# Kernel tuning notes

Hardware: AMD Instinct MI355X
Metric: run time of the kernel (lower is better)

Reference implementation:

```python
import jax, jax.numpy as jnp
import numpy as np

N_NODES = 50000
N_EDGES = 800000
D = 128
L = 4
N_GRAPHS = 512
N_CLASSES = 10
BN_EPS = 1e-5


def setup_inputs() -> dict:
    key = jax.random.key(0)
    ks = jax.random.split(key, 8)
    x = jax.random.normal(ks[0], (N_NODES, D), dtype=jnp.float32)
    W = jax.random.normal(ks[1], (L, D, D), dtype=jnp.float32) * (1.0 / np.sqrt(D))
    b = jnp.zeros((L, D), dtype=jnp.float32)
    gamma = jnp.ones((L, D), dtype=jnp.float32)
    beta = jnp.zeros((L, D), dtype=jnp.float32)
    Wc = jax.random.normal(ks[2], (D, N_CLASSES), dtype=jnp.float32) * (1.0 / np.sqrt(D))
    bc = jnp.zeros((N_CLASSES,), dtype=jnp.float32)
    edge_index = jax.random.randint(ks[3], (2, N_EDGES), 0, N_NODES, dtype=jnp.int64)
    batch = jnp.sort(jax.random.randint(ks[4], (N_NODES,), 0, N_GRAPHS, dtype=jnp.int64))
    return {"x": x, "W": W, "b": b, "gamma": gamma, "beta": beta,
            "Wc": Wc, "bc": bc, "edge_index": edge_index, "batch": batch}


def _gcn_conv(x, W_l, b_l, src, dst, deg_inv, norm):
    # h = x @ W, then symmetric-normalized aggregation with self-loops (PyG GCNConv)
    h = x @ W_l                                            # [N, D]
    msg = h[src] * norm[:, None]                           # [E, D] gather + scale
    agg = jax.ops.segment_sum(msg, dst, num_segments=N_NODES)  # scatter-add
    agg = agg + h * (deg_inv * deg_inv)[:, None]           # self-loop term: deg^-1 * h_i
    return agg + b_l


def reference(x, W, b, gamma, beta, Wc, bc, edge_index, batch):
    src, dst = edge_index[0], edge_index[1]
    # degree with self-loops (edge_weight = 1), computed at target nodes
    deg = jax.ops.segment_sum(jnp.ones((N_EDGES,), x.dtype), dst, num_segments=N_NODES) + 1.0
    deg_inv = deg ** -0.5                                  # [N]
    norm = deg_inv[src] * deg_inv[dst]                     # [E]
    for l in range(L):
        x = _gcn_conv(x, W[l], b[l], src, dst, deg_inv, norm)
        # BatchNorm1d (training-mode statistics, biased variance) + ReLU
        mu = jnp.mean(x, axis=0)
        var = jnp.mean((x - mu) ** 2, axis=0)
        x = (x - mu) * jax.lax.rsqrt(var + BN_EPS) * gamma[l] + beta[l]
        x = jax.nn.relu(x)
        # dropout omitted (eval-mode / deterministic reference)
    # global mean pool over graphs, then classifier
    sums = jax.ops.segment_sum(x, batch, num_segments=N_GRAPHS)          # [G, D]
    counts = jax.ops.segment_sum(jnp.ones((N_NODES,), x.dtype), batch, num_segments=N_GRAPHS)
    pooled = sums / jnp.maximum(counts, 1.0)[:, None]
    return pooled @ Wc + bc                                # [G, num_classes]
```

## Files before the change

kernel.cpp:

```cpp
#include <hip/hip_runtime.h>
#include <hip/hip_bf16.h>

#define N_NODES 50000
#define N_EDGES 800000
#define D 128
#define NLAYERS 4
#define N_GRAPHS 512
#define N_CLASSES 10
#define BN_EPS 1e-5f
#define SCAN_BLOCKS ((N_NODES + 1023) / 1024)
#define NPART 64

__global__ void k_hist(const int* __restrict__ ei, int* __restrict__ counts) {
    int e = blockIdx.x * blockDim.x + threadIdx.x;
    if (e < N_EDGES) atomicAdd(&counts[ei[N_EDGES + e]], 1);
}

__global__ __launch_bounds__(1024) void k_scan1(const int* __restrict__ counts,
                                                int* __restrict__ offsets,
                                                float* __restrict__ deg_inv,
                                                int* __restrict__ bsum) {
    __shared__ int wsum[16];
    int tid = threadIdx.x, lane = tid & 63, wid = tid >> 6;
    int i = blockIdx.x * 1024 + tid;
    int v = (i < N_NODES) ? counts[i] : 0;
    if (i < N_NODES) deg_inv[i] = rsqrtf((float)v + 1.0f);
    int x = v;
    #pragma unroll
    for (int off = 1; off < 64; off <<= 1) {
        int y = __shfl_up(x, off, 64);
        if (lane >= off) x += y;
    }
    if (lane == 63) wsum[wid] = x;
    __syncthreads();
    if (wid == 0 && lane < 16) {
        int w = wsum[lane];
        #pragma unroll
        for (int off = 1; off < 16; off <<= 1) {
            int y = __shfl_up(w, off, 16);
            if (lane >= off) w += y;
        }
        wsum[lane] = w;
    }
    __syncthreads();
    int wbase = (wid > 0) ? wsum[wid - 1] : 0;
    int incl = x + wbase;
    if (i < N_NODES) offsets[i + 1] = incl;
    if (tid == 1023) bsum[blockIdx.x] = incl;
}

__global__ __launch_bounds__(1024) void k_scan2(int* __restrict__ offsets,
                                                const int* __restrict__ bsum) {
    __shared__ int s_pre;
    int b = blockIdx.x, tid = threadIdx.x;
    if (tid == 0) {
        int p = 0;
        for (int j = 0; j < b; j++) p += bsum[j];
        s_pre = p;
        if (b == 0) offsets[0] = 0;
    }
    __syncthreads();
    int i = b * 1024 + tid;
    if (i < N_NODES) offsets[i + 1] += s_pre;
}

__global__ void k_scatter(const int* __restrict__ ei, const int* __restrict__ offsets,
                          int* __restrict__ cursor, const float* __restrict__ deg_inv,
                          int2* __restrict__ csr) {
    int e = blockIdx.x * blockDim.x + threadIdx.x;
    if (e >= N_EDGES) return;
    int s = ei[e];
    int d = ei[N_EDGES + e];
    int pos = offsets[d] + atomicAdd(&cursor[d], 1);
    csr[pos] = make_int2(s, __float_as_int(deg_inv[s] * deg_inv[d]));
}

#define GEMM_BM 64
__global__ __launch_bounds__(256) void k_gemm(const float* __restrict__ X,
                                              const float* __restrict__ Wl,
                                              float* __restrict__ H,
                                              const float* __restrict__ gstats,
                                              const float* __restrict__ gamma,
                                              const float* __restrict__ beta,
                                              int do_bn_relu) {
    __shared__ float xs[GEMM_BM][D];
    __shared__ float s_sc[D], s_sh[D];
    int tid = threadIdx.x;
    if (tid < D) {
        if (do_bn_relu) {
            float s = 0.f, q = 0.f;
            #pragma unroll 8
            for (int p = 0; p < NPART; p++) {
                s += gstats[p * 2 * D + tid];
                q += gstats[p * 2 * D + D + tid];
            }
            const float invN = 1.0f / (float)N_NODES;
            float mu = s * invN;
            float var = q * invN - mu * mu;
            float sc = gamma[tid] * rsqrtf(var + BN_EPS);
            s_sc[tid] = sc;
            s_sh[tid] = beta[tid] - mu * sc;
        } else {
            s_sc[tid] = 1.0f;
            s_sh[tid] = 0.0f;
        }
    }
    __syncthreads();
    int row0 = blockIdx.x * GEMM_BM;
    #pragma unroll
    for (int j = 0; j < 8; j++) {
        int idx = tid + j * 256;
        int r = idx >> 5;
        int c4 = (idx & 31) * 4;
        float4 v;
        int gr = row0 + r;
        if (gr < N_NODES) v = *(const float4*)&X[(long)gr * D + c4];
        else v = make_float4(0.f, 0.f, 0.f, 0.f);
        if (do_bn_relu) {
            v.x = fmaxf(v.x * s_sc[c4 + 0] + s_sh[c4 + 0], 0.f);
            v.y = fmaxf(v.y * s_sc[c4 + 1] + s_sh[c4 + 1], 0.f);
            v.z = fmaxf(v.z * s_sc[c4 + 2] + s_sh[c4 + 2], 0.f);
            v.w = fmaxf(v.w * s_sc[c4 + 3] + s_sh[c4 + 3], 0.f);
        }
        *(float4*)&xs[r][c4] = v;
    }
    __syncthreads();
    int tc = tid & 31, tr = tid >> 5;
    int r0 = tr * 8, c0 = tc * 4;
    float acc[8][4] = {};
    #pragma unroll 4
    for (int k = 0; k < D; k++) {
        float4 w = *(const float4*)&Wl[k * D + c0];
        #pragma unroll
        for (int i = 0; i < 8; i++) {
            float xv = xs[r0 + i][k];
            acc[i][0] += xv * w.x;
            acc[i][1] += xv * w.y;
            acc[i][2] += xv * w.z;
            acc[i][3] += xv * w.w;
        }
    }
    #pragma unroll
    for (int i = 0; i < 8; i++) {
        int gr = row0 + r0 + i;
        if (gr < N_NODES) {
            float4 o = make_float4(acc[i][0], acc[i][1], acc[i][2], acc[i][3]);
            *(float4*)&H[(long)gr * D + c0] = o;
        }
    }
}

#define AGG_NPW 2
#define AGG_WAVES 4
#define AGG_NPB (AGG_NPW * AGG_WAVES)
__global__ __launch_bounds__(256) void k_agg(const float* __restrict__ H,
                                             const float* __restrict__ deg_inv,
                                             const int* __restrict__ offsets,
                                             const int2* __restrict__ csr,
                                             const float* __restrict__ bias,
                                             float* __restrict__ Xout,
                                             float* __restrict__ gstats) {
    __shared__ float s_sum[D], s_sq[D];
    int tid = threadIdx.x, lane = tid & 63, wid = tid >> 6;
    if (tid < D) { s_sum[tid] = 0.f; s_sq[tid] = 0.f; }
    __syncthreads();
    int c = lane * 2;
    float b0 = bias[c], b1 = bias[c + 1];
    float ps0 = 0.f, ps1 = 0.f, pq0 = 0.f, pq1 = 0.f;
    int nodeBase = blockIdx.x * AGG_NPB + wid * AGG_NPW;
    for (int t = 0; t < AGG_NPW; t++) {
        int n = nodeBase + t;
        if (n >= N_NODES) break;
        float di = deg_inv[n];
        float2 hv = *(const float2*)&H[(long)n * D + c];
        float self = di * di;
        float a0 = hv.x * self + b0;
        float a1 = hv.y * self + b1;
        int e = offsets[n], e1 = offsets[n + 1];
        for (; e + 4 <= e1; e += 4) {
            int2 p0 = csr[e + 0];
            int2 p1 = csr[e + 1];
            int2 p2 = csr[e + 2];
            int2 p3 = csr[e + 3];
            float2 h0 = *(const float2*)&H[(long)p0.x * D + c];
            float2 h1 = *(const float2*)&H[(long)p1.x * D + c];
            float2 h2 = *(const float2*)&H[(long)p2.x * D + c];
            float2 h3 = *(const float2*)&H[(long)p3.x * D + c];
            float w0 = __int_as_float(p0.y), w1 = __int_as_float(p1.y);
            float w2 = __int_as_float(p2.y), w3 = __int_as_float(p3.y);
            a0 += h0.x * w0; a1 += h0.y * w0;
            a0 += h1.x * w1; a1 += h1.y * w1;
            a0 += h2.x * w2; a1 += h2.y * w2;
            a0 += h3.x * w3; a1 += h3.y * w3;
        }
        for (; e < e1; e++) {
            int2 p = csr[e];
            float w = __int_as_float(p.y);
            float2 hs = *(const float2*)&H[(long)p.x * D + c];
            a0 += hs.x * w;
            a1 += hs.y * w;
        }
        *(float2*)&Xout[(long)n * D + c] = make_float2(a0, a1);
        ps0 += a0; ps1 += a1;
        pq0 += a0 * a0; pq1 += a1 * a1;
    }
    atomicAdd(&s_sum[c], ps0);
    atomicAdd(&s_sum[c + 1], ps1);
    atomicAdd(&s_sq[c], pq0);
    atomicAdd(&s_sq[c + 1], pq1);
    __syncthreads();
    if (tid < D) {
        int part = blockIdx.x & (NPART - 1);
        float* gp = gstats + (size_t)part * 2 * D;
        atomicAdd(&gp[tid], s_sum[tid]);
        atomicAdd(&gp[D + tid], s_sq[tid]);
    }
}

__global__ __launch_bounds__(256) void k_poolcls(const float* __restrict__ X,
                                                 const int* __restrict__ batch,
                                                 const float* __restrict__ gstats,
                                                 const float* __restrict__ gamma,
                                                 const float* __restrict__ beta,
                                                 const float* __restrict__ Wc,
                                                 const float* __restrict__ bc,
                                                 float* __restrict__ out) {
    __shared__ float s_pool[D];
    __shared__ float s_sc[D], s_sh[D];
    __shared__ int s_lo, s_hi;
    int g = blockIdx.x, tid = threadIdx.x;
    if (tid == 0) {
        int lo = 0, hi = N_NODES;
        while (lo < hi) { int m = (lo + hi) >> 1; if (batch[m] < g) lo = m + 1; else hi = m; }
        s_lo = lo;
        hi = N_NODES;
        while (lo < hi) { int m = (lo + hi) >> 1; if (batch[m] < g + 1) lo = m + 1; else hi = m; }
        s_hi = lo;
    }
    if (tid < D) {
        float s = 0.f, q = 0.f;
        #pragma unroll 8
        for (int p = 0; p < NPART; p++) {
            s += gstats[p * 2 * D + tid];
            q += gstats[p * 2 * D + D + tid];
        }
        const float invN = 1.0f / (float)N_NODES;
        float mu = s * invN;
        float var = q * invN - mu * mu;
        float sc = gamma[tid] * rsqrtf(var + BN_EPS);
        s_sc[tid] = sc;
        s_sh[tid] = beta[tid] - mu * sc;
        s_pool[tid] = 0.f;
    }
    __syncthreads();
    int lo = s_lo, hi = s_hi;
    int c4 = (tid & 31) * 4, q = tid >> 5;
    float sc[4], sh[4];
    #pragma unroll
    for (int j = 0; j < 4; j++) { sc[j] = s_sc[c4 + j]; sh[j] = s_sh[c4 + j]; }
    float acc[4] = {0.f, 0.f, 0.f, 0.f};
    for (int n = lo + q; n < hi; n += 8) {
        float4 v = *(const float4*)&X[(long)n * D + c4];
        acc[0] += fmaxf(v.x * sc[0] + sh[0], 0.f);
        acc[1] += fmaxf(v.y * sc[1] + sh[1], 0.f);
        acc[2] += fmaxf(v.z * sc[2] + sh[2], 0.f);
        acc[3] += fmaxf(v.w * sc[3] + sh[3], 0.f);
    }
    #pragma unroll
    for (int j = 0; j < 4; j++) atomicAdd(&s_pool[c4 + j], acc[j]);
    __syncthreads();
    if (tid < N_CLASSES) {
        float cnt = fmaxf((float)(hi - lo), 1.0f);
        float r = 0.f;
        #pragma unroll 16
        for (int k = 0; k < D; k++) r += s_pool[k] * Wc[k * N_CLASSES + tid];
        out[(long)g * N_CLASSES + tid] = r / cnt + bc[tid];
    }
}

extern "C" void kernel_launch(void* const* d_in, const int* in_sizes, int n_in,
                              void* d_out, int out_size, void* d_ws, size_t ws_size,
                              hipStream_t stream) {
    const float* x     = (const float*)d_in[0];
    const float* W     = (const float*)d_in[1];
    const float* b     = (const float*)d_in[2];
    const float* gamma = (const float*)d_in[3];
    const float* beta  = (const float*)d_in[4];
    const float* Wc    = (const float*)d_in[5];
    const float* bc    = (const float*)d_in[6];
    const int*   ei    = (const int*)d_in[7];
    const int*   batch = (const int*)d_in[8];
    float* out = (float*)d_out;

    char* ws = (char*)d_ws;
    size_t off = 0;
    auto alloc = [&](size_t bytes) {
        void* p = ws + off;
        off += (bytes + 255) & ~(size_t)255;
        return p;
    };
    float* cur_x    = (float*)alloc((size_t)N_NODES * D * 4);
    float* h        = (float*)alloc((size_t)N_NODES * D * 4);
    float* deg_inv  = (float*)alloc(N_NODES * 4);
    int*   offsets  = (int*)alloc((N_NODES + 1) * 4);
    int2*  csr      = (int2*)alloc((size_t)N_EDGES * 8);
    int*   bsum     = (int*)alloc(SCAN_BLOCKS * 4);
    size_t zero_begin = off;
    int*   counts   = (int*)alloc(N_NODES * 4);
    int*   cursor   = (int*)alloc(N_NODES * 4);
    float* gstats   = (float*)alloc((size_t)NLAYERS * NPART * 2 * D * 4);
    size_t zero_end = off;

    hipMemsetAsync(ws + zero_begin, 0, zero_end - zero_begin, stream);

    k_hist<<<(N_EDGES + 255) / 256, 256, 0, stream>>>(ei, counts);
    k_scan1<<<SCAN_BLOCKS, 1024, 0, stream>>>(counts, offsets, deg_inv, bsum);
    k_scan2<<<SCAN_BLOCKS, 1024, 0, stream>>>(offsets, bsum);
    k_scatter<<<(N_EDGES + 255) / 256, 256, 0, stream>>>(ei, offsets, cursor, deg_inv, csr);

    const int gemm_grid = (N_NODES + GEMM_BM - 1) / GEMM_BM;
    const int agg_grid = (N_NODES + AGG_NPB - 1) / AGG_NPB;
    const size_t lstat = (size_t)NPART * 2 * D;
    for (int l = 0; l < NLAYERS; l++) {
        const float* Xin = (l == 0) ? x : cur_x;
        const float* st  = (l == 0) ? nullptr : gstats + (size_t)(l - 1) * lstat;
        const float* gm  = gamma + (size_t)((l == 0) ? 0 : l - 1) * D;
        const float* bt  = beta + (size_t)((l == 0) ? 0 : l - 1) * D;
        k_gemm<<<gemm_grid, 256, 0, stream>>>(Xin, W + (size_t)l * D * D, h,
                                              st, gm, bt, (l == 0) ? 0 : 1);
        k_agg<<<agg_grid, 256, 0, stream>>>(h, deg_inv, offsets, csr,
                                            b + (size_t)l * D, cur_x,
                                            gstats + (size_t)l * lstat);
    }

    k_poolcls<<<N_GRAPHS, 256, 0, stream>>>(cur_x, batch,
                                            gstats + (size_t)(NLAYERS - 1) * lstat,
                                            gamma + (size_t)(NLAYERS - 1) * D,
                                            beta + (size_t)(NLAYERS - 1) * D,
                                            Wc, bc, out);
}
```

Measured before the change: 633.9 us.

## Store H in column-chunked layout and aggregate per feature chunk

The GEMM now writes H as 8 column chunks of 16 features, each stored contiguously per node. Aggregation blocks handle one chunk, with a wave splitting edges across 4 slots and combining them by shuffle reduction, so each chunk (3.2 MB) is more likely to stay cache-resident during the random gathers. The cost is that each CSR row is re-read once per chunk, and each gather only fetches 64 bytes per edge. The grid assumes N_NODES is divisible by 16, and the node bounds check has been removed.

```diff
diff --git a/kernel.cpp b/kernel.cpp
--- a/kernel.cpp
+++ b/kernel.cpp
@@ -10,6 +10,8 @@
 #define BN_EPS 1e-5f
 #define SCAN_BLOCKS ((N_NODES + 1023) / 1024)
 #define NPART 64
+#define NCHUNK 8
+#define CHUNKW 16
 
 __global__ void k_hist(const int* __restrict__ ei, int* __restrict__ counts) {
     int e = blockIdx.x * blockDim.x + threadIdx.x;
@@ -78,7 +80,7 @@
 #define GEMM_BM 64
 __global__ __launch_bounds__(256) void k_gemm(const float* __restrict__ X,
                                               const float* __restrict__ Wl,
-                                              float* __restrict__ H,
+                                              float* __restrict__ Hc,
                                               const float* __restrict__ gstats,
                                               const float* __restrict__ gamma,
                                               const float* __restrict__ beta,
@@ -140,80 +142,82 @@
             acc[i][3] += xv * w.w;
         }
     }
+    int chunk = c0 >> 4;
+    int within = c0 & 15;
     #pragma unroll
     for (int i = 0; i < 8; i++) {
         int gr = row0 + r0 + i;
         if (gr < N_NODES) {
             float4 o = make_float4(acc[i][0], acc[i][1], acc[i][2], acc[i][3]);
-            *(float4*)&H[(long)gr * D + c0] = o;
-        }
-    }
-}
-
-#define AGG_NPW 2
-#define AGG_WAVES 4
-#define AGG_NPB (AGG_NPW * AGG_WAVES)
-__global__ __launch_bounds__(256) void k_agg(const float* __restrict__ H,
+            *(float4*)&Hc[(size_t)chunk * N_NODES * CHUNKW + (size_t)gr * CHUNKW + within] = o;
+        }
+    }
+}
+
+#define AGGC_NPW 4
+#define AGGC_WAVES 4
+#define AGGC_NPB (AGGC_NPW * AGGC_WAVES)
+__global__ __launch_bounds__(256) void k_agg(const float* __restrict__ Hc,
                                              const float* __restrict__ deg_inv,
                                              const int* __restrict__ offsets,
                                              const int2* __restrict__ csr,
                                              const float* __restrict__ bias,
                                              float* __restrict__ Xout,
                                              float* __restrict__ gstats) {
-    __shared__ float s_sum[D], s_sq[D];
+    __shared__ float s_sum[CHUNKW], s_sq[CHUNKW];
     int tid = threadIdx.x, lane = tid & 63, wid = tid >> 6;
-    if (tid < D) { s_sum[tid] = 0.f; s_sq[tid] = 0.f; }
-    __syncthreads();
-    int c = lane * 2;
-    float b0 = bias[c], b1 = bias[c + 1];
-    float ps0 = 0.f, ps1 = 0.f, pq0 = 0.f, pq1 = 0.f;
-    int nodeBase = blockIdx.x * AGG_NPB + wid * AGG_NPW;
-    for (int t = 0; t < AGG_NPW; t++) {
-        int n = nodeBase + t;
-        if (n >= N_NODES) break;
-        float di = deg_inv[n];
-        float2 hv = *(const float2*)&H[(long)n * D + c];
-        float self = di * di;
-        float a0 = hv.x * self + b0;
-        float a1 = hv.y * self + b1;
+    int bid = blockIdx.x;
+    int chunk = bid & (NCHUNK - 1);
+    int grp = bid >> 3;
+    if (tid < CHUNKW) { s_sum[tid] = 0.f; s_sq[tid] = 0.f; }
+    __syncthreads();
+    const float* Hbase = Hc + (size_t)chunk * N_NODES * CHUNKW;
+    int col = lane & 15;
+    int slot = lane >> 4;
+    float b = bias[chunk * CHUNKW + col];
+    float ps = 0.f, pq = 0.f;
+    int n0 = grp * AGGC_NPB + wid * AGGC_NPW;
+    for (int t = 0; t < AGGC_NPW; t++) {
+        int n = n0 + t;
+        float a = 0.f;
         int e = offsets[n], e1 = offsets[n + 1];
-        for (; e + 4 <= e1; e += 4) {
-            int2 p0 = csr[e + 0];
-            int2 p1 = csr[e + 1];
-            int2 p2 = csr[e + 2];
-            int2 p3 = csr[e + 3];
-            float2 h0 = *(const float2*)&H[(long)p0.x * D + c];
-            float2 h1 = *(const float2*)&H[(long)p1.x * D + c];
-            float2 h2 = *(const float2*)&H[(long)p2.x * D + c];
-            float2 h3 = *(const float2*)&H[(long)p3.x * D + c];
-            float w0 = __int_as_float(p0.y), w1 = __int_as_float(p1.y);
-            float w2 = __int_as_float(p2.y), w3 = __int_as_float(p3.y);
-            a0 += h0.x * w0; a1 += h0.y * w0;
-            a0 += h1.x * w1; a1 += h1.y * w1;
-            a0 += h2.x * w2; a1 += h2.y * w2;
-            a0 += h3.x * w3; a1 += h3.y * w3;
-        }
-        for (; e < e1; e++) {
-            int2 p = csr[e];
-            float w = __int_as_float(p.y);
-            float2 hs = *(const float2*)&H[(long)p.x * D + c];
-            a0 += hs.x * w;
-            a1 += hs.y * w;
-        }
-        *(float2*)&Xout[(long)n * D + c] = make_float2(a0, a1);
-        ps0 += a0; ps1 += a1;
-        pq0 += a0 * a0; pq1 += a1 * a1;
-    }
-    atomicAdd(&s_sum[c], ps0);
-    atomicAdd(&s_sum[c + 1], ps1);
-    atomicAdd(&s_sq[c], pq0);
-    atomicAdd(&s_sq[c + 1], pq1);
-    __syncthreads();
-    if (tid < D) {
-        int part = blockIdx.x & (NPART - 1);
+        for (; e + 8 <= e1; e += 8) {
+            long long v0 = __builtin_nontemporal_load((const long long*)&csr[e + slot]);
+            long long v1 = __builtin_nontemporal_load((const long long*)&csr[e + 4 + slot]);
+            int src0 = (int)v0; float w0 = __int_as_float((int)(v0 >> 32));
+            int src1 = (int)v1; float w1 = __int_as_float((int)(v1 >> 32));
+            float h0 = Hbase[(size_t)src0 * CHUNKW + col];
+            float h1 = Hbase[(size_t)src1 * CHUNKW + col];
+            a += h0 * w0 + h1 * w1;
+        }
+        for (; e < e1; e += 4) {
+            int ee = e + slot;
+            if (ee < e1) {
+                long long v = __builtin_nontemporal_load((const long long*)&csr[ee]);
+                int src = (int)v; float w = __int_as_float((int)(v >> 32));
+                a += Hbase[(size_t)src * CHUNKW + col] * w;
+            }
+        }
+        a += __shfl_xor(a, 16, 64);
+        a += __shfl_xor(a, 32, 64);
+        if (slot == 0) {
+            float di = deg_inv[n];
+            float r = a + Hbase[(size_t)n * CHUNKW + col] * (di * di) + b;
+            __builtin_nontemporal_store(r, &Xout[(size_t)n * D + chunk * CHUNKW + col]);
+            ps += r;
+            pq += r * r;
+        }
+    }
+    if (slot == 0) {
+        atomicAdd(&s_sum[col], ps);
+        atomicAdd(&s_sq[col], pq);
+    }
+    __syncthreads();
+    if (tid < CHUNKW) {
+        int part = grp & (NPART - 1);
         float* gp = gstats + (size_t)part * 2 * D;
-        atomicAdd(&gp[tid], s_sum[tid]);
-        atomicAdd(&gp[D + tid], s_sq[tid]);
+        atomicAdd(&gp[chunk * CHUNKW + tid], s_sum[tid]);
+        atomicAdd(&gp[D + chunk * CHUNKW + tid], s_sq[tid]);
     }
 }
 
@@ -319,7 +323,7 @@
     k_scatter<<<(N_EDGES + 255) / 256, 256, 0, stream>>>(ei, offsets, cursor, deg_inv, csr);
 
     const int gemm_grid = (N_NODES + GEMM_BM - 1) / GEMM_BM;
-    const int agg_grid = (N_NODES + AGG_NPB - 1) / AGG_NPB;
+    const int agg_grid = (N_NODES / AGGC_NPB) * NCHUNK;
     const size_t lstat = (size_t)NPART * 2 * D;
     for (int l = 0; l < NLAYERS; l++) {
         const float* Xin = (l == 0) ? x : cur_x;
```

Measured after the change: 1.087 ms. 71.4% more time.
